# Optimization experiments

Measured on AMD Instinct MI355X. Metric: run time of the kernel, lower is better.

## Reference

```python
import jax, jax.numpy as jnp
import numpy as np

B, N, H, D, K, HEADS = 128, 64, 256, 128, 8, 3


def _ln(x, g, b):
    mu = x.mean(-1, keepdims=True)
    var = x.var(-1, keepdims=True)
    return (x - mu) * jax.lax.rsqrt(var + 1e-5) * g + b


def _mmlp2(x, W1, b1, g1, be1, W2, b2):
    # per-node batched MLP: [B,N,in] x [N,in,out] -> [B,N,out]
    h = jnp.einsum('bni,nio->bno', x, W1) + b1
    h = jax.nn.relu(_ln(h, g1, be1))
    return jnp.einsum('bni,nio->bno', h, W2) + b2


def _chi(x, m1, m2):
    # 2-additive Mobius Choquet integral, averaged over heads.
    # x: [B,S,K,D], m1: [S,heads,K] (singleton Mobius), m2: [S,heads,K,K] (pair Mobius, upper-tri)
    tri = jnp.triu(jnp.ones((K, K), x.dtype), k=1)
    pairmin = jnp.minimum(x[:, :, :, None, :], x[:, :, None, :, :])  # [B,S,K,K,D]
    single = jnp.einsum('shk,bskd->bsd', m1, x)
    pair = jnp.einsum('shij,bsijd->bsd', m2 * tri, pairmin)
    return (single + pair) / HEADS


def setup_inputs() -> dict:
    key = jax.random.key(0)
    ks = jax.random.split(key, 10)
    s = lambda k, *sh: (jax.random.normal(k, sh, jnp.float32) * 0.05)
    inp = {}
    inp['observation'] = jax.random.normal(ks[0], (B, N, H), jnp.float32)
    inp['action'] = jax.random.normal(ks[1], (B, N, H), jnp.float32)
    inp['local_edges'] = jax.random.randint(ks[2], (N, 2, K + 1), 0, N)
    inp['V_W1'] = s(ks[3], N, H, H);   inp['V_b1'] = jnp.zeros((N, H), jnp.float32)
    inp['V_g1'] = jnp.ones((H,), jnp.float32); inp['V_beta1'] = jnp.zeros((H,), jnp.float32)
    inp['V_W2'] = s(ks[4], N, H, D);   inp['V_b2'] = jnp.zeros((N, D), jnp.float32)
    inp['A_W1'] = s(ks[5], N, 2 * H, H); inp['A_b1'] = jnp.zeros((N, H), jnp.float32)
    inp['A_g1'] = jnp.ones((H,), jnp.float32); inp['A_beta1'] = jnp.zeros((H,), jnp.float32)
    inp['A_W2'] = s(ks[6], N, H, D);   inp['A_b2'] = jnp.zeros((N, D), jnp.float32)
    inp['chi_m1'] = s(ks[7], N, HEADS, K)
    inp['chi_m2'] = s(ks[8], N, HEADS, K, K)
    return inp


def reference(observation, action, local_edges, V_W1, V_b1, V_g1, V_beta1, V_W2, V_b2,
              A_W1, A_b1, A_g1, A_beta1, A_W2, A_b2, chi_m1, chi_m2):
    V = _mmlp2(observation, V_W1, V_b1, V_g1, V_beta1, V_W2, V_b2)          # [B,N,D]
    A = _mmlp2(jnp.concatenate([observation, action], -1),
               A_W1, A_b1, A_g1, A_beta1, A_W2, A_b2)                       # [B,N,D]
    Q = A + V
    centers = local_edges[:, 0, 0]   # [S]
    neigh = local_edges[:, 0, 1:]    # [S,K]
    # .data in torch detaches the gathered neighbors
    Qn = jax.lax.stop_gradient(Q[:, neigh, :])   # [B,S,K,D]
    Vn = jax.lax.stop_gradient(V[:, neigh, :])
    chi_q = (_chi(Qn, chi_m1, chi_m2) + Q[:, centers, :]).mean(-1)  # [B,S]
    chi_v = (_chi(Vn, chi_m1, chi_m2) + V[:, centers, :]).mean(-1)  # [B,S]
    return chi_q, chi_v
```

## Files before the change

### kernel.cpp

```cpp
#include <hip/hip_runtime.h>
#include <hip/hip_bf16.h>

#define BCNT 128
#define NNODE 64
#define HDIM 256
#define DDIM 128
#define KNEI 8
#define NR (BCNT * NNODE)

#define OFF1V 0ull
#define OFF1A 4194304ull
#define OFF2V 12582912ull
#define OFF2A 14680064ull
#define WTOT  16777216ull
#define XPL   2097152ull

typedef __attribute__((ext_vector_type(8))) short bf16x8;
typedef __attribute__((ext_vector_type(8))) unsigned short ushort8;
typedef __attribute__((ext_vector_type(16))) float f32x16;

__device__ __forceinline__ unsigned short f2bf(float f) {
    union { __hip_bfloat16 b; unsigned short u; } c;
    c.b = __float2bfloat16(f);
    return c.u;
}
__device__ __forceinline__ float bf2f(unsigned short u) {
    union { unsigned short u; __hip_bfloat16 b; } c;
    c.u = u;
    return __bfloat162float(c.b);
}
__device__ __forceinline__ void split2(float f, unsigned short& h, unsigned short& l) {
    h = f2bf(f);
    l = f2bf(f - bf2f(h));
}

__global__ __launch_bounds__(256) void xsplit_frag(
    const float* __restrict__ obs, const float* __restrict__ act,
    ushort* __restrict__ obsH, ushort* __restrict__ obsL,
    ushort* __restrict__ actH, ushort* __restrict__ actL)
{
    const int bx = blockIdx.x;
    const int n = bx >> 2, bt = bx & 3;
    const int srcsel = blockIdx.y;
    const float* S = srcsel ? act : obs;
    ushort* DH = srcsel ? actH : obsH;
    ushort* DL = srcsel ? actL : obsL;

    __shared__ float tile[32 * 257];
    const int t = threadIdx.x;
    {
        const int r = t >> 3, cg = (t & 7) * 32;
        const float* row = S + ((size_t)(bt * 32 + r) * NNODE + n) * HDIM + cg;
        #pragma unroll
        for (int j = 0; j < 8; ++j) {
            float4 v = *(const float4*)(row + j * 4);
            tile[r * 257 + cg + j * 4 + 0] = v.x;
            tile[r * 257 + cg + j * 4 + 1] = v.y;
            tile[r * 257 + cg + j * 4 + 2] = v.z;
            tile[r * 257 + cg + j * 4 + 3] = v.w;
        }
    }
    __syncthreads();
    const int lane = t & 63, g = t >> 6;
    #pragma unroll
    for (int jj = 0; jj < 4; ++jj) {
        const int kt = g * 4 + jj;
        ushort8 h8, l8;
        #pragma unroll
        for (int i = 0; i < 8; ++i) {
            float v = tile[(lane & 31) * 257 + kt * 16 + (lane >> 5) * 8 + i];
            unsigned short hh, ll; split2(v, hh, ll);
            h8[i] = hh; l8[i] = ll;
        }
        size_t idx = ((((size_t)n * 4 + bt) * 16 + kt) * 64 + lane) * 8;
        *(ushort8*)(DH + idx) = h8;
        *(ushort8*)(DL + idx) = l8;
    }
}

__global__ __launch_bounds__(256) void wsplit_frag(
    const float* __restrict__ VW1, const float* __restrict__ AW1,
    const float* __restrict__ VW2, const float* __restrict__ AW2,
    ushort* __restrict__ WFH, ushort* __restrict__ WFL)
{
    const int n = blockIdx.y;
    const int tt = blockIdx.x;
    const float* src; size_t fb; int OUT, KT, tk, to;
    if (tt < 16)      { src = VW1 + (size_t)n * 65536;  fb = OFF1V / 512 + (size_t)n * 8 * 16; OUT = 256; KT = 16; tk = tt >> 2;        to = tt & 3;        }
    else if (tt < 48) { src = AW1 + (size_t)n * 131072; fb = OFF1A / 512 + (size_t)n * 8 * 32; OUT = 256; KT = 32; tk = (tt - 16) >> 2; to = (tt - 16) & 3; }
    else if (tt < 56) { src = VW2 + (size_t)n * 32768;  fb = OFF2V / 512 + (size_t)n * 4 * 16; OUT = 128; KT = 16; tk = (tt - 48) >> 1; to = (tt - 48) & 1; }
    else              { src = AW2 + (size_t)n * 32768;  fb = OFF2A / 512 + (size_t)n * 4 * 16; OUT = 128; KT = 16; tk = (tt - 56) >> 1; to = (tt - 56) & 1; }

    const int k0 = tk * 64, o0 = to * 64;
    __shared__ float tile[64 * 65];
    const int t = threadIdx.x;
    {
        const int r = t >> 2, cg = (t & 3) * 16;
        const float* row = src + (size_t)(k0 + r) * OUT + o0 + cg;
        #pragma unroll
        for (int j = 0; j < 4; ++j) {
            float4 v = *(const float4*)(row + j * 4);
            tile[r * 65 + cg + j * 4 + 0] = v.x;
            tile[r * 65 + cg + j * 4 + 1] = v.y;
            tile[r * 65 + cg + j * 4 + 2] = v.z;
            tile[r * 65 + cg + j * 4 + 3] = v.w;
        }
    }
    __syncthreads();
    const int lane = t & 63, g = t >> 6;
    const int ol = g >> 1;
    #pragma unroll
    for (int jj = 0; jj < 2; ++jj) {
        const int kl = (g & 1) * 2 + jj;
        ushort8 h8, l8;
        #pragma unroll
        for (int i = 0; i < 8; ++i) {
            float v = tile[(kl * 16 + (lane >> 5) * 8 + i) * 65 + ol * 32 + (lane & 31)];
            unsigned short hh, ll; split2(v, hh, ll);
            h8[i] = hh; l8[i] = ll;
        }
        size_t fi = fb + (size_t)(to * 2 + ol) * KT + (size_t)(tk * 4 + kl);
        size_t idx = (fi * 64 + lane) * 8;
        *(ushort8*)(WFH + idx) = h8;
        *(ushort8*)(WFL + idx) = l8;
    }
}

__global__ __launch_bounds__(512, 4) void fused_mlp(
    const ushort* __restrict__ obsH, const ushort* __restrict__ obsL,
    const ushort* __restrict__ actH, const ushort* __restrict__ actL,
    const ushort* __restrict__ WFH, const ushort* __restrict__ WFL,
    const float* __restrict__ Vb1, const float* __restrict__ Ab1,
    const float* __restrict__ Vg1, const float* __restrict__ Vbe1,
    const float* __restrict__ Ag1, const float* __restrict__ Abe1,
    const float* __restrict__ Vb2, const float* __restrict__ Ab2,
    float* __restrict__ Vout, float* __restrict__ Aout)
{
    const int id = blockIdx.x;
    const int xcd = id & 7, slot = id >> 3;
    const int bt = slot & 3;
    const int pair = (slot >> 2) * 8 + xcd;
    const int n = pair >> 1, br = pair & 1;

    const int t = threadIdx.x;
    const int l = t & 63, w = t >> 6;
    const int lo = l & 31, gg = l >> 5;

    __shared__ ushort hbtH[32 * 264];
    __shared__ ushort hbtL[32 * 264];
    __shared__ float2 lnS[8][32];
    __shared__ float2 lnp[32];
    __shared__ float red[4][16][64];

    const int nkt = br ? 32 : 16;
    const size_t wb = (br ? OFF1A + ((size_t)n * 8 + w) * 32 * 512
                          : OFF1V + ((size_t)n * 8 + w) * 16 * 512) + (size_t)l * 8;
    const size_t xb = (((size_t)n * 4 + bt) * 16) * 512 + (size_t)l * 8;

    f32x16 aP = {}, aQ = {};
    #pragma unroll 4
    for (int kt = 0; kt < nkt; ++kt) {
        const ushort* xh; const ushort* xl;
        if (br && kt >= 16) { xh = actH; xl = actL; }
        else                { xh = obsH; xl = obsL; }
        const size_t xi = xb + (size_t)(kt & 15) * 512;
        const size_t wi = wb + (size_t)kt * 512;
        bf16x8 ah = *(const bf16x8*)(xh + xi);
        bf16x8 al = *(const bf16x8*)(xl + xi);
        bf16x8 bh = *(const bf16x8*)(WFH + wi);
        bf16x8 bl = *(const bf16x8*)(WFL + wi);
        aP = __builtin_amdgcn_mfma_f32_32x32x16_bf16(ah, bh, aP, 0, 0, 0);
        aQ = __builtin_amdgcn_mfma_f32_32x32x16_bf16(ah, bl, aQ, 0, 0, 0);
        aQ = __builtin_amdgcn_mfma_f32_32x32x16_bf16(al, bh, aQ, 0, 0, 0);
    }

    const int col = w * 32 + lo;
    const float b1 = (br ? Ab1 : Vb1)[n * HDIM + col];
    float v[16];
    #pragma unroll
    for (int r = 0; r < 16; ++r) {
        v[r] = aP[r] + aQ[r] + b1;
        float s = v[r], q = v[r] * v[r];
        #pragma unroll
        for (int off = 1; off < 32; off <<= 1) {
            s += __shfl_xor(s, off);
            q += __shfl_xor(q, off);
        }
        if (lo == 0) lnS[w][(r & 3) + 8 * (r >> 2) + 4 * gg] = float2{s, q};
    }
    __syncthreads();
    if (t < 32) {
        float ss = 0.f, qq = 0.f;
        #pragma unroll
        for (int w2 = 0; w2 < 8; ++w2) { ss += lnS[w2][t].x; qq += lnS[w2][t].y; }
        float mu = ss * (1.0f / 256.0f);
        float var = qq * (1.0f / 256.0f) - mu * mu;
        lnp[t] = float2{mu, rsqrtf(var + 1e-5f)};
    }
    __syncthreads();
    {
        const float g1 = (br ? Ag1 : Vg1)[col];
        const float be = (br ? Abe1 : Vbe1)[col];
        #pragma unroll
        for (int r = 0; r < 16; ++r) {
            const int mm = (r & 3) + 8 * (r >> 2) + 4 * gg;
            float2 p = lnp[mm];
            float y = fmaxf((v[r] - p.x) * p.y * g1 + be, 0.0f);
            unsigned short hh, ll; split2(y, hh, ll);
            hbtH[mm * 264 + col] = hh;
            hbtL[mm * 264 + col] = ll;
        }
    }
    __syncthreads();

    const int ot2 = w & 3, kh = w >> 2;
    const size_t w2b = (br ? OFF2A : OFF2V) + ((size_t)n * 4 + ot2) * 16 * 512 + (size_t)l * 8;
    f32x16 cP = {}, cQ = {};
    #pragma unroll
    for (int j = 0; j < 8; ++j) {
        const int kt = kh * 8 + j;
        const int lb = lo * 264 + kt * 16 + gg * 8;
        bf16x8 ah = *(const bf16x8*)&hbtH[lb];
        bf16x8 al = *(const bf16x8*)&hbtL[lb];
        const size_t wi = w2b + (size_t)kt * 512;
        bf16x8 bh = *(const bf16x8*)(WFH + wi);
        bf16x8 bl = *(const bf16x8*)(WFL + wi);
        cP = __builtin_amdgcn_mfma_f32_32x32x16_bf16(ah, bh, cP, 0, 0, 0);
        cQ = __builtin_amdgcn_mfma_f32_32x32x16_bf16(ah, bl, cQ, 0, 0, 0);
        cQ = __builtin_amdgcn_mfma_f32_32x32x16_bf16(al, bh, cQ, 0, 0, 0);
    }
    float c[16];
    #pragma unroll
    for (int r = 0; r < 16; ++r) c[r] = cP[r] + cQ[r];
    if (w >= 4) {
        #pragma unroll
        for (int r = 0; r < 16; ++r) red[w - 4][r][l] = c[r];
    }
    __syncthreads();
    if (w < 4) {
        const float b2 = (br ? Ab2 : Vb2)[n * DDIM + ot2 * 32 + lo];
        float* outp = br ? Aout : Vout;
        #pragma unroll
        for (int r = 0; r < 16; ++r) {
            const int mm = (r & 3) + 8 * (r >> 2) + 4 * gg;
            outp[((size_t)(bt * 32 + mm) * NNODE + n) * DDIM + ot2 * 32 + lo]
                = c[r] + red[w][r][l] + b2;
        }
    }
}

__global__ __launch_bounds__(128) void chi_kernel(
    const float* __restrict__ V, const float* __restrict__ A,
    const int* __restrict__ le, const float* __restrict__ m1,
    const float* __restrict__ m2, float* __restrict__ out)
{
    const int n = blockIdx.x;
    const int b = blockIdx.y;
    const int tid = threadIdx.x;

    __shared__ float sm1[KNEI];
    __shared__ float sm2[KNEI * KNEI];
    __shared__ int   sidx[KNEI + 1];
    __shared__ float pq[2], pv[2];

    if (tid < KNEI) {
        float s = 0.0f;
        #pragma unroll
        for (int hh = 0; hh < 3; ++hh) s += m1[n * 24 + hh * 8 + tid];
        sm1[tid] = s;
    }
    if (tid < 64) {
        int i = tid >> 3, j = tid & 7;
        float s = 0.0f;
        if (j > i) {
            #pragma unroll
            for (int hh = 0; hh < 3; ++hh) s += m2[n * 192 + hh * 64 + tid];
        }
        sm2[tid] = s;
    }
    if (tid < KNEI + 1) sidx[tid] = le[n * 18 + tid];
    __syncthreads();

    const float* Vb_ = V + (size_t)b * (NNODE * DDIM);
    const float* Ab_ = A + (size_t)b * (NNODE * DDIM);
    const int cen = sidx[0];

    float vn[KNEI], qn[KNEI];
    #pragma unroll
    for (int k = 0; k < KNEI; ++k) {
        int nb = sidx[1 + k];
        float vv = Vb_[nb * DDIM + tid];
        float aa = Ab_[nb * DDIM + tid];
        vn[k] = vv;
        qn[k] = vv + aa;
    }

    float sq = 0.0f, sv = 0.0f;
    #pragma unroll
    for (int k = 0; k < KNEI; ++k) { sq += sm1[k] * qn[k]; sv += sm1[k] * vn[k]; }
    #pragma unroll
    for (int i = 0; i < KNEI; ++i) {
        #pragma unroll
        for (int j = i + 1; j < KNEI; ++j) {
            float w = sm2[i * 8 + j];
            sq += w * fminf(qn[i], qn[j]);
            sv += w * fminf(vn[i], vn[j]);
        }
    }

    float Vc = Vb_[cen * DDIM + tid];
    float Ac = Ab_[cen * DDIM + tid];
    float valq = sq * (1.0f / 3.0f) + (Vc + Ac);
    float valv = sv * (1.0f / 3.0f) + Vc;

    #pragma unroll
    for (int o = 32; o; o >>= 1) {
        valq += __shfl_down(valq, o);
        valv += __shfl_down(valv, o);
    }
    if ((tid & 63) == 0) { pq[tid >> 6] = valq; pv[tid >> 6] = valv; }
    __syncthreads();
    if (tid == 0) {
        out[b * NNODE + n]                = (pq[0] + pq[1]) * (1.0f / 128.0f);
        out[BCNT * NNODE + b * NNODE + n] = (pv[0] + pv[1]) * (1.0f / 128.0f);
    }
}

extern "C" void kernel_launch(void* const* d_in, const int* in_sizes, int n_in,
                              void* d_out, int out_size, void* d_ws, size_t ws_size,
                              hipStream_t stream)
{
    const float* obs  = (const float*)d_in[0];
    const float* act  = (const float*)d_in[1];
    const int*   le   = (const int*)  d_in[2];
    const float* VW1  = (const float*)d_in[3];
    const float* Vb1  = (const float*)d_in[4];
    const float* Vg1  = (const float*)d_in[5];
    const float* Vbe1 = (const float*)d_in[6];
    const float* VW2  = (const float*)d_in[7];
    const float* Vb2  = (const float*)d_in[8];
    const float* AW1  = (const float*)d_in[9];
    const float* Ab1  = (const float*)d_in[10];
    const float* Ag1  = (const float*)d_in[11];
    const float* Abe1 = (const float*)d_in[12];
    const float* AW2  = (const float*)d_in[13];
    const float* Ab2  = (const float*)d_in[14];
    const float* m1   = (const float*)d_in[15];
    const float* m2   = (const float*)d_in[16];
    float* out = (float*)d_out;

    ushort* WFH  = (ushort*)d_ws;
    ushort* WFL  = WFH + WTOT;
    ushort* obsH = WFL + WTOT;
    ushort* obsL = obsH + XPL;
    ushort* actH = obsL + XPL;
    ushort* actL = actH + XPL;
    float*  V    = (float*)(actL + XPL);
    float*  A    = V + (size_t)NR * DDIM;

    wsplit_frag<<<dim3(64, 64), dim3(256), 0, stream>>>(VW1, AW1, VW2, AW2, WFH, WFL);
    xsplit_frag<<<dim3(256, 2), dim3(256), 0, stream>>>(obs, act, obsH, obsL, actH, actL);
    fused_mlp<<<dim3(512), dim3(512), 0, stream>>>(obsH, obsL, actH, actL, WFH, WFL,
                                                   Vb1, Ab1, Vg1, Vbe1, Ag1, Abe1,
                                                   Vb2, Ab2, V, A);
    chi_kernel<<<dim3(NNODE, BCNT), dim3(128), 0, stream>>>(V, A, le, m1, m2, out);
}
```

Before: 198.7 us.

## Fuse weight bf16 splitting into MLP kernel and switch to 16x16 MFMA tiles

Removes the separate weight pre-split kernel and its workspace. The fused MLP now reads fp32 weights directly and splits them into hi/lo bf16 in registers. It switches from 32x32x16 to 16x16x32 MFMA with 16-row batch tiles, doubling the grid to 1024 blocks and raising the occupancy hint. The aim is to save the extra weight read/write pass and a launch. The cost is strided scalar fp32 weight loads and duplicated split work across the 8 batch tiles that each re-read the weights.

```diff
diff --git a/kernel.cpp b/kernel.cpp
--- a/kernel.cpp
+++ b/kernel.cpp
@@ -7,17 +7,11 @@
 #define DDIM 128
 #define KNEI 8
 #define NR (BCNT * NNODE)
-
-#define OFF1V 0ull
-#define OFF1A 4194304ull
-#define OFF2V 12582912ull
-#define OFF2A 14680064ull
-#define WTOT  16777216ull
-#define XPL   2097152ull
+#define XPL 2097152ull
 
 typedef __attribute__((ext_vector_type(8))) short bf16x8;
 typedef __attribute__((ext_vector_type(8))) unsigned short ushort8;
-typedef __attribute__((ext_vector_type(16))) float f32x16;
+typedef __attribute__((ext_vector_type(4))) float f32x4;
 
 __device__ __forceinline__ unsigned short f2bf(float f) {
     union { __hip_bfloat16 b; unsigned short u; } c;
@@ -40,96 +34,50 @@
     ushort* __restrict__ actH, ushort* __restrict__ actL)
 {
     const int bx = blockIdx.x;
-    const int n = bx >> 2, bt = bx & 3;
-    const int srcsel = blockIdx.y;
-    const float* S = srcsel ? act : obs;
-    ushort* DH = srcsel ? actH : obsH;
-    ushort* DL = srcsel ? actL : obsL;
-
-    __shared__ float tile[32 * 257];
+    const int n = bx >> 3, bt = bx & 7;
+    const float* S = blockIdx.y ? act : obs;
+    ushort* DH = blockIdx.y ? actH : obsH;
+    ushort* DL = blockIdx.y ? actL : obsL;
+
+    __shared__ float tile[16][257];
     const int t = threadIdx.x;
     {
-        const int r = t >> 3, cg = (t & 7) * 32;
-        const float* row = S + ((size_t)(bt * 32 + r) * NNODE + n) * HDIM + cg;
-        #pragma unroll
-        for (int j = 0; j < 8; ++j) {
+        const int r = t >> 4, cs = (t & 15) * 16;
+        const float* row = S + ((size_t)(bt * 16 + r) * NNODE + n) * HDIM + cs;
+        #pragma unroll
+        for (int j = 0; j < 4; ++j) {
             float4 v = *(const float4*)(row + j * 4);
-            tile[r * 257 + cg + j * 4 + 0] = v.x;
-            tile[r * 257 + cg + j * 4 + 1] = v.y;
-            tile[r * 257 + cg + j * 4 + 2] = v.z;
-            tile[r * 257 + cg + j * 4 + 3] = v.w;
-        }
-    }
-    __syncthreads();
-    const int lane = t & 63, g = t >> 6;
-    #pragma unroll
-    for (int jj = 0; jj < 4; ++jj) {
-        const int kt = g * 4 + jj;
+            tile[r][cs + j * 4 + 0] = v.x;
+            tile[r][cs + j * 4 + 1] = v.y;
+            tile[r][cs + j * 4 + 2] = v.z;
+            tile[r][cs + j * 4 + 3] = v.w;
+        }
+    }
+    __syncthreads();
+    const int kt = t >> 5, sub = t & 31;
+    const int row = sub & 15;
+    #pragma unroll
+    for (int lg = 0; lg < 2; ++lg) {
+        const int lane = lg * 32 + sub;
+        const int kg = lane >> 4;
         ushort8 h8, l8;
         #pragma unroll
         for (int i = 0; i < 8; ++i) {
-            float v = tile[(lane & 31) * 257 + kt * 16 + (lane >> 5) * 8 + i];
-            unsigned short hh, ll; split2(v, hh, ll);
+            unsigned short hh, ll;
+            split2(tile[row][kt * 32 + kg * 8 + i], hh, ll);
             h8[i] = hh; l8[i] = ll;
         }
-        size_t idx = ((((size_t)n * 4 + bt) * 16 + kt) * 64 + lane) * 8;
+        size_t idx = ((((size_t)n * 8 + bt) * 8 + kt) * 512) + (size_t)lane * 8;
         *(ushort8*)(DH + idx) = h8;
         *(ushort8*)(DL + idx) = l8;
     }
 }
 
-__global__ __launch_bounds__(256) void wsplit_frag(
+__global__ __launch_bounds__(512, 6) void fused_mlp(
+    const ushort* __restrict__ obsH, const ushort* __restrict__ obsL,
+    const ushort* __restrict__ actH, const ushort* __restrict__ actL,
     const float* __restrict__ VW1, const float* __restrict__ AW1,
     const float* __restrict__ VW2, const float* __restrict__ AW2,
-    ushort* __restrict__ WFH, ushort* __restrict__ WFL)
-{
-    const int n = blockIdx.y;
-    const int tt = blockIdx.x;
-    const float* src; size_t fb; int OUT, KT, tk, to;
-    if (tt < 16)      { src = VW1 + (size_t)n * 65536;  fb = OFF1V / 512 + (size_t)n * 8 * 16; OUT = 256; KT = 16; tk = tt >> 2;        to = tt & 3;        }
-    else if (tt < 48) { src = AW1 + (size_t)n * 131072; fb = OFF1A / 512 + (size_t)n * 8 * 32; OUT = 256; KT = 32; tk = (tt - 16) >> 2; to = (tt - 16) & 3; }
-    else if (tt < 56) { src = VW2 + (size_t)n * 32768;  fb = OFF2V / 512 + (size_t)n * 4 * 16; OUT = 128; KT = 16; tk = (tt - 48) >> 1; to = (tt - 48) & 1; }
-    else              { src = AW2 + (size_t)n * 32768;  fb = OFF2A / 512 + (size_t)n * 4 * 16; OUT = 128; KT = 16; tk = (tt - 56) >> 1; to = (tt - 56) & 1; }
-
-    const int k0 = tk * 64, o0 = to * 64;
-    __shared__ float tile[64 * 65];
-    const int t = threadIdx.x;
-    {
-        const int r = t >> 2, cg = (t & 3) * 16;
-        const float* row = src + (size_t)(k0 + r) * OUT + o0 + cg;
-        #pragma unroll
-        for (int j = 0; j < 4; ++j) {
-            float4 v = *(const float4*)(row + j * 4);
-            tile[r * 65 + cg + j * 4 + 0] = v.x;
-            tile[r * 65 + cg + j * 4 + 1] = v.y;
-            tile[r * 65 + cg + j * 4 + 2] = v.z;
-            tile[r * 65 + cg + j * 4 + 3] = v.w;
-        }
-    }
-    __syncthreads();
-    const int lane = t & 63, g = t >> 6;
-    const int ol = g >> 1;
-    #pragma unroll
-    for (int jj = 0; jj < 2; ++jj) {
-        const int kl = (g & 1) * 2 + jj;
-        ushort8 h8, l8;
-        #pragma unroll
-        for (int i = 0; i < 8; ++i) {
-            float v = tile[(kl * 16 + (lane >> 5) * 8 + i) * 65 + ol * 32 + (lane & 31)];
-            unsigned short hh, ll; split2(v, hh, ll);
-            h8[i] = hh; l8[i] = ll;
-        }
-        size_t fi = fb + (size_t)(to * 2 + ol) * KT + (size_t)(tk * 4 + kl);
-        size_t idx = (fi * 64 + lane) * 8;
-        *(ushort8*)(WFH + idx) = h8;
-        *(ushort8*)(WFL + idx) = l8;
-    }
-}
-
-__global__ __launch_bounds__(512, 4) void fused_mlp(
-    const ushort* __restrict__ obsH, const ushort* __restrict__ obsL,
-    const ushort* __restrict__ actH, const ushort* __restrict__ actL,
-    const ushort* __restrict__ WFH, const ushort* __restrict__ WFL,
     const float* __restrict__ Vb1, const float* __restrict__ Ab1,
     const float* __restrict__ Vg1, const float* __restrict__ Vbe1,
     const float* __restrict__ Ag1, const float* __restrict__ Abe1,
@@ -137,59 +85,80 @@
     float* __restrict__ Vout, float* __restrict__ Aout)
 {
     const int id = blockIdx.x;
-    const int xcd = id & 7, slot = id >> 3;
-    const int bt = slot & 3;
-    const int pair = (slot >> 2) * 8 + xcd;
+    const int bt = id >> 7;
+    const int pair = id & 127;
     const int n = pair >> 1, br = pair & 1;
 
     const int t = threadIdx.x;
     const int l = t & 63, w = t >> 6;
-    const int lo = l & 31, gg = l >> 5;
-
-    __shared__ ushort hbtH[32 * 264];
-    __shared__ ushort hbtL[32 * 264];
-    __shared__ float2 lnS[8][32];
-    __shared__ float2 lnp[32];
-    __shared__ float red[4][16][64];
-
-    const int nkt = br ? 32 : 16;
-    const size_t wb = (br ? OFF1A + ((size_t)n * 8 + w) * 32 * 512
-                          : OFF1V + ((size_t)n * 8 + w) * 16 * 512) + (size_t)l * 8;
-    const size_t xb = (((size_t)n * 4 + bt) * 16) * 512 + (size_t)l * 8;
-
-    f32x16 aP = {}, aQ = {};
-    #pragma unroll 4
+    const int l16 = l & 15, g4 = l >> 4;
+
+    __shared__ ushort hbtH[16 * 264];
+    __shared__ ushort hbtL[16 * 264];
+    __shared__ float2 lnS[8][16];
+    __shared__ float2 lnp[16];
+
+    const int nkt = br ? 16 : 8;
+    const float* W1n = br ? (AW1 + (size_t)n * 512 * HDIM)
+                          : (VW1 + (size_t)n * 256 * HDIM);
+    const int col0 = w * 32 + l16;
+    const int col1 = w * 32 + 16 + l16;
+
+    f32x4 aP0 = {}, aQ0 = {}, aP1 = {}, aQ1 = {};
+    #pragma unroll 2
     for (int kt = 0; kt < nkt; ++kt) {
         const ushort* xh; const ushort* xl;
-        if (br && kt >= 16) { xh = actH; xl = actL; }
-        else                { xh = obsH; xl = obsL; }
-        const size_t xi = xb + (size_t)(kt & 15) * 512;
-        const size_t wi = wb + (size_t)kt * 512;
+        if (br && kt >= 8) { xh = actH; xl = actL; }
+        else               { xh = obsH; xl = obsL; }
+        const size_t xi = ((((size_t)n * 8 + bt) * 8 + (kt & 7)) * 512) + (size_t)l * 8;
         bf16x8 ah = *(const bf16x8*)(xh + xi);
         bf16x8 al = *(const bf16x8*)(xl + xi);
-        bf16x8 bh = *(const bf16x8*)(WFH + wi);
-        bf16x8 bl = *(const bf16x8*)(WFL + wi);
-        aP = __builtin_amdgcn_mfma_f32_32x32x16_bf16(ah, bh, aP, 0, 0, 0);
-        aQ = __builtin_amdgcn_mfma_f32_32x32x16_bf16(ah, bl, aQ, 0, 0, 0);
-        aQ = __builtin_amdgcn_mfma_f32_32x32x16_bf16(al, bh, aQ, 0, 0, 0);
-    }
-
-    const int col = w * 32 + lo;
-    const float b1 = (br ? Ab1 : Vb1)[n * HDIM + col];
-    float v[16];
-    #pragma unroll
-    for (int r = 0; r < 16; ++r) {
-        v[r] = aP[r] + aQ[r] + b1;
-        float s = v[r], q = v[r] * v[r];
-        #pragma unroll
-        for (int off = 1; off < 32; off <<= 1) {
-            s += __shfl_xor(s, off);
-            q += __shfl_xor(q, off);
-        }
-        if (lo == 0) lnS[w][(r & 3) + 8 * (r >> 2) + 4 * gg] = float2{s, q};
-    }
-    __syncthreads();
-    if (t < 32) {
+
+        const float* wk = W1n + (size_t)(kt * 32 + g4 * 8) * HDIM;
+        bf16x8 bh0, bl0, bh1, bl1;
+        #pragma unroll
+        for (int i = 0; i < 8; ++i) {
+            unsigned short hh, ll;
+            split2(wk[(size_t)i * HDIM + col0], hh, ll);
+            bh0[i] = (short)hh; bl0[i] = (short)ll;
+            split2(wk[(size_t)i * HDIM + col1], hh, ll);
+            bh1[i] = (short)hh; bl1[i] = (short)ll;
+        }
+        aP0 = __builtin_amdgcn_mfma_f32_16x16x32_bf16(ah, bh0, aP0, 0, 0, 0);
+        aQ0 = __builtin_amdgcn_mfma_f32_16x16x32_bf16(ah, bl0, aQ0, 0, 0, 0);
+        aQ0 = __builtin_amdgcn_mfma_f32_16x16x32_bf16(al, bh0, aQ0, 0, 0, 0);
+        aP1 = __builtin_amdgcn_mfma_f32_16x16x32_bf16(ah, bh1, aP1, 0, 0, 0);
+        aQ1 = __builtin_amdgcn_mfma_f32_16x16x32_bf16(ah, bl1, aQ1, 0, 0, 0);
+        aQ1 = __builtin_amdgcn_mfma_f32_16x16x32_bf16(al, bh1, aQ1, 0, 0, 0);
+    }
+
+    const float* b1p = (br ? Ab1 : Vb1) + (size_t)n * HDIM;
+    const float bc0 = b1p[col0], bc1 = b1p[col1];
+    float v0[4], v1[4];
+    {
+        float s[4], q[4];
+        #pragma unroll
+        for (int j = 0; j < 4; ++j) {
+            v0[j] = aP0[j] + aQ0[j] + bc0;
+            v1[j] = aP1[j] + aQ1[j] + bc1;
+            s[j] = v0[j] + v1[j];
+            q[j] = v0[j] * v0[j] + v1[j] * v1[j];
+        }
+        #pragma unroll
+        for (int off = 1; off < 16; off <<= 1) {
+            #pragma unroll
+            for (int j = 0; j < 4; ++j) {
+                s[j] += __shfl_xor(s[j], off);
+                q[j] += __shfl_xor(q[j], off);
+            }
+        }
+        if (l16 == 0) {
+            #pragma unroll
+            for (int j = 0; j < 4; ++j) lnS[w][g4 * 4 + j] = float2{s[j], q[j]};
+        }
+    }
+    __syncthreads();
+    if (t < 16) {
         float ss = 0.f, qq = 0.f;
         #pragma unroll
         for (int w2 = 0; w2 < 8; ++w2) { ss += lnS[w2][t].x; qq += lnS[w2][t].y; }
@@ -199,52 +168,52 @@
     }
     __syncthreads();
     {
-        const float g1 = (br ? Ag1 : Vg1)[col];
-        const float be = (br ? Abe1 : Vbe1)[col];
-        #pragma unroll
-        for (int r = 0; r < 16; ++r) {
-            const int mm = (r & 3) + 8 * (r >> 2) + 4 * gg;
-            float2 p = lnp[mm];
-            float y = fmaxf((v[r] - p.x) * p.y * g1 + be, 0.0f);
-            unsigned short hh, ll; split2(y, hh, ll);
-            hbtH[mm * 264 + col] = hh;
-            hbtL[mm * 264 + col] = ll;
-        }
-    }
-    __syncthreads();
-
-    const int ot2 = w & 3, kh = w >> 2;
-    const size_t w2b = (br ? OFF2A : OFF2V) + ((size_t)n * 4 + ot2) * 16 * 512 + (size_t)l * 8;
-    f32x16 cP = {}, cQ = {};
-    #pragma unroll
-    for (int j = 0; j < 8; ++j) {
-        const int kt = kh * 8 + j;
-        const int lb = lo * 264 + kt * 16 + gg * 8;
+        const float* gp = br ? Ag1 : Vg1;
+        const float* bep = br ? Abe1 : Vbe1;
+        const float g0 = gp[col0], g1 = gp[col1];
+        const float e0 = bep[col0], e1 = bep[col1];
+        #pragma unroll
+        for (int j = 0; j < 4; ++j) {
+            const int row = g4 * 4 + j;
+            float2 p = lnp[row];
+            float y0 = fmaxf((v0[j] - p.x) * p.y * g0 + e0, 0.0f);
+            float y1 = fmaxf((v1[j] - p.x) * p.y * g1 + e1, 0.0f);
+            unsigned short hh, ll;
+            split2(y0, hh, ll);
+            hbtH[row * 264 + col0] = hh; hbtL[row * 264 + col0] = ll;
+            split2(y1, hh, ll);
+            hbtH[row * 264 + col1] = hh; hbtL[row * 264 + col1] = ll;
+        }
+    }
+    __syncthreads();
+
+    const float* W2n = (br ? AW2 : VW2) + (size_t)n * HDIM * DDIM;
+    const int ocol = w * 16 + l16;
+    f32x4 cP = {}, cQ = {};
+    #pragma unroll 2
+    for (int kt = 0; kt < 8; ++kt) {
+        const int lb = l16 * 264 + kt * 32 + g4 * 8;
         bf16x8 ah = *(const bf16x8*)&hbtH[lb];
         bf16x8 al = *(const bf16x8*)&hbtL[lb];
-        const size_t wi = w2b + (size_t)kt * 512;
-        bf16x8 bh = *(const bf16x8*)(WFH + wi);
-        bf16x8 bl = *(const bf16x8*)(WFL + wi);
-        cP = __builtin_amdgcn_mfma_f32_32x32x16_bf16(ah, bh, cP, 0, 0, 0);
-        cQ = __builtin_amdgcn_mfma_f32_32x32x16_bf16(ah, bl, cQ, 0, 0, 0);
-        cQ = __builtin_amdgcn_mfma_f32_32x32x16_bf16(al, bh, cQ, 0, 0, 0);
-    }
-    float c[16];
-    #pragma unroll
-    for (int r = 0; r < 16; ++r) c[r] = cP[r] + cQ[r];
-    if (w >= 4) {
-        #pragma unroll
-        for (int r = 0; r < 16; ++r) red[w - 4][r][l] = c[r];
-    }
-    __syncthreads();
-    if (w < 4) {
-        const float b2 = (br ? Ab2 : Vb2)[n * DDIM + ot2 * 32 + lo];
+        const float* wk = W2n + (size_t)(kt * 32 + g4 * 8) * DDIM;
+        bf16x8 bh, bl;
+        #pragma unroll
+        for (int i = 0; i < 8; ++i) {
+            unsigned short hh, ll;
+            split2(wk[(size_t)i * DDIM + ocol], hh, ll);
+            bh[i] = (short)hh; bl[i] = (short)ll;
+        }
+        cP = __builtin_amdgcn_mfma_f32_16x16x32_bf16(ah, bh, cP, 0, 0, 0);
+        cQ = __builtin_amdgcn_mfma_f32_16x16x32_bf16(ah, bl, cQ, 0, 0, 0);
+        cQ = __builtin_amdgcn_mfma_f32_16x16x32_bf16(al, bh, cQ, 0, 0, 0);
+    }
+    {
+        const float b2 = (br ? Ab2 : Vb2)[(size_t)n * DDIM + ocol];
         float* outp = br ? Aout : Vout;
         #pragma unroll
-        for (int r = 0; r < 16; ++r) {
-            const int mm = (r & 3) + 8 * (r >> 2) + 4 * gg;
-            outp[((size_t)(bt * 32 + mm) * NNODE + n) * DDIM + ot2 * 32 + lo]
-                = c[r] + red[w][r][l] + b2;
+        for (int j = 0; j < 4; ++j) {
+            const int brow = bt * 16 + g4 * 4 + j;
+            outp[((size_t)brow * NNODE + n) * DDIM + ocol] = cP[j] + cQ[j] + b2;
         }
     }
 }
@@ -349,19 +318,17 @@
     const float* m2   = (const float*)d_in[16];
     float* out = (float*)d_out;
 
-    ushort* WFH  = (ushort*)d_ws;
-    ushort* WFL  = WFH + WTOT;
-    ushort* obsH = WFL + WTOT;
+    ushort* obsH = (ushort*)d_ws;
     ushort* obsL = obsH + XPL;
     ushort* actH = obsL + XPL;
     ushort* actL = actH + XPL;
     float*  V    = (float*)(actL + XPL);
     float*  A    = V + (size_t)NR * DDIM;
 
-    wsplit_frag<<<dim3(64, 64), dim3(256), 0, stream>>>(VW1, AW1, VW2, AW2, WFH, WFL);
-    xsplit_frag<<<dim3(256, 2), dim3(256), 0, stream>>>(obs, act, obsH, obsL, actH, actL);
-    fused_mlp<<<dim3(512), dim3(512), 0, stream>>>(obsH, obsL, actH, actL, WFH, WFL,
-                                                   Vb1, Ab1, Vg1, Vbe1, Ag1, Abe1,
-                                                   Vb2, Ab2, V, A);
+    xsplit_frag<<<dim3(512, 2), dim3(256), 0, stream>>>(obs, act, obsH, obsL, actH, actL);
+    fused_mlp<<<dim3(1024), dim3(512), 0, stream>>>(obsH, obsL, actH, actL,
+                                                    VW1, AW1, VW2, AW2,
+                                                    Vb1, Ab1, Vg1, Vbe1, Ag1, Abe1,
+                                                    Vb2, Ab2, V, A);
     chi_kernel<<<dim3(NNODE, BCNT), dim3(128), 0, stream>>>(V, A, le, m1, m2, out);
 }
```

After: 188.6 us. 1.05x faster.
